# Kernel tuning notes

Hardware: AMD Instinct MI355X
Metric: run time of the kernel (lower is better)

The kernel has to match this reference:

```python
import jax, jax.numpy as jnp
import numpy as np
import math

B, N, F = 16, 1024, 2048


def setup_inputs() -> dict:
    key = jax.random.key(0)
    k_t, k_y = jax.random.split(key)
    # sorted time samples in [0, 100) per batch row
    t = jnp.sort(jax.random.uniform(k_t, (B, N), dtype=jnp.float32) * 100.0, axis=-1)
    y = jax.random.normal(k_y, (B, N), dtype=jnp.float32)
    mask = jnp.ones((B, N), dtype=jnp.float32)
    # monotonically increasing frequency grid (torch.diff in norm requires this)
    freqs = jnp.linspace(1e-5, 5.0, F, dtype=jnp.float32)
    return {"t": t, "y": y, "mask": mask, "freqs": freqs}


def reference(t, y, mask, freqs):
    # t, y, mask: (B, N); freqs: (F,)
    two_pi = 2.0 * math.pi
    omega = two_pi * freqs  # (F,)
    w = omega[None, :, None]          # (1, F, 1)
    tb = t[:, None, :]                # (B, 1, N)
    mb = mask[:, None, :]             # (B, 1, N)
    yb = y[:, None, :]                # (B, 1, N)

    # --- stage 1: tau per (batch, freq) ---
    two_wt = 2.0 * w * tb             # (B, F, N)
    s_sum = jnp.sum(jnp.sin(two_wt) * mb, axis=-1)  # (B, F)
    c_sum = jnp.sum(jnp.cos(two_wt) * mb, axis=-1)  # (B, F)
    tau = jnp.arctan2(s_sum, c_sum) / (2.0 * omega)  # (B, F)

    # --- stage 2: power ---
    wt_tau = w * (tb - tau[:, :, None])  # (B, F, N)
    cos_term = jnp.cos(wt_tau) * mb
    sin_term = jnp.sin(wt_tau) * mb
    p_cos = jnp.sum(yb * cos_term, axis=-1) ** 2 / (jnp.sum(cos_term * cos_term, axis=-1) + 1e-10)
    p_sin = jnp.sum(yb * sin_term, axis=-1) ** 2 / (jnp.sum(sin_term * sin_term, axis=-1) + 1e-10)
    p = 0.5 * (p_cos + p_sin)  # (B, F)

    # --- FAP weighting ---
    m = p.shape[-1]
    fap = 1.0 - (1.0 - jnp.exp(-p)) ** m
    p = p * (1.0 / (fap + 1e-5))

    # --- trapezoidal normalization over the freq grid ---
    df = jnp.diff(freqs)  # (F-1,)
    integral = jnp.sum(0.5 * (p[:, :-1] + p[:, 1:]) * df, axis=-1) + 1e-10  # (B,)
    return p / integral[:, None]
```

## Files before the change

### kernel.cpp

```cpp
#include <hip/hip_runtime.h>
#include <math.h>

#define B_ 16
#define N_ 1024
#define F_ 2048
#define FPB 64
#define SLICES 16
#define NS (N_ / SLICES)
#define NC (NS / 4)

typedef float v2f __attribute__((ext_vector_type(2)));

__global__ __launch_bounds__(1024, 8) void ls_power_kernel(
    const float* __restrict__ t,
    const float* __restrict__ y,
    const float* __restrict__ mask,
    const float* __restrict__ freqs,
    float* __restrict__ p_out)
{
    const int tid   = threadIdx.x;
    const int fi    = tid & (FPB - 1);
    const int slice = tid >> 6;
    const int b     = blockIdx.y;
    const int f     = blockIdx.x * FPB + fi;

    const float freq = freqs[f];
    const v2f  fq2  = {freq, freq};
    const v2f  onev = {1.0f, 1.0f};
    const v2f  ntwo = {-2.0f, -2.0f};

    __shared__ float4 sh[3 * (N_ / 4)];
    if (tid < 3 * (N_ / 4)) {
        const int a = tid >> 8;
        const int i = tid & (N_ / 4 - 1);
        const float4* __restrict__ src =
            (a == 0) ? (const float4*)t : (a == 1) ? (const float4*)y
                                                   : (const float4*)mask;
        sh[tid] = src[b * (N_ / 4) + i];
    }

    __shared__ float red[SLICES][7][FPB];
    __syncthreads();

    const float4* __restrict__ sh_t = sh;
    const float4* __restrict__ sh_y = sh + (N_ / 4);
    const float4* __restrict__ sh_m = sh + 2 * (N_ / 4);
    const int c0 = slice * NC;

    v2f S = {0.f, 0.f}, C = S, S2 = S, C2 = S, Sy = S, Cy = S, M2 = S;

    auto pair = [&](float ta, float tb, float ya, float yb, float ma, float mb) {
        v2f tn = {ta, tb}, yn = {ya, yb}, mn = {ma, mb};
        v2f ph = fq2 * tn;
        v2f pe = __builtin_elementwise_fma(fq2, tn, -ph);
        v2f fr = {__builtin_amdgcn_fractf(ph.x),
                  __builtin_amdgcn_fractf(ph.y)};
        v2f r  = fr + pe;
        v2f s0 = {__builtin_amdgcn_sinf(r.x), __builtin_amdgcn_sinf(r.y)};
        v2f c0v = {__builtin_amdgcn_cosf(r.x), __builtin_amdgcn_cosf(r.y)};
        v2f t1 = s0 * c0v;
        v2f s2v = t1 + t1;
        v2f w  = s0 * s0;
        v2f c2v = __builtin_elementwise_fma(w, ntwo, onev);
        v2f m2v = mn * mn;
        v2f ymv = yn * mn;
        S  = __builtin_elementwise_fma(s2v, mn,  S);
        C  = __builtin_elementwise_fma(c2v, mn,  C);
        S2 = __builtin_elementwise_fma(s2v, m2v, S2);
        C2 = __builtin_elementwise_fma(c2v, m2v, C2);
        Sy = __builtin_elementwise_fma(s0,  ymv, Sy);
        Cy = __builtin_elementwise_fma(c0v, ymv, Cy);
        M2 = M2 + m2v;
    };

#pragma unroll 2
    for (int ch = 0; ch < NC; ++ch) {
        float4 tv = sh_t[c0 + ch];
        float4 yv = sh_y[c0 + ch];
        float4 mv = sh_m[c0 + ch];
        pair(tv.x, tv.y, yv.x, yv.y, mv.x, mv.y);
        pair(tv.z, tv.w, yv.z, yv.w, mv.z, mv.w);
    }

    red[slice][0][fi] = S.x  + S.y;
    red[slice][1][fi] = C.x  + C.y;
    red[slice][2][fi] = S2.x + S2.y;
    red[slice][3][fi] = C2.x + C2.y;
    red[slice][4][fi] = Sy.x + Sy.y;
    red[slice][5][fi] = Cy.x + Cy.y;
    red[slice][6][fi] = M2.x + M2.y;
    __syncthreads();

    if (slice == 0) {
        float rS = 0.f, rC = 0.f, rS2 = 0.f, rC2 = 0.f, rSy = 0.f, rCy = 0.f, rM2 = 0.f;
#pragma unroll
        for (int k = 0; k < SLICES; ++k) {
            rS  += red[k][0][fi];
            rC  += red[k][1][fi];
            rS2 += red[k][2][fi];
            rC2 += red[k][3][fi];
            rSy += red[k][4][fi];
            rCy += red[k][5][fi];
            rM2 += red[k][6][fi];
        }

        float h      = sqrtf(__builtin_fmaf(rS, rS, rC * rC)) + 1e-30f;
        float cos2p  = rC / h;
        float sin2p  = rS / h;
        float cosp   = sqrtf(0.5f * (1.0f + cos2p));
        float sinp   = __builtin_copysignf(sqrtf(0.5f * (1.0f - cos2p)), rS);

        float YC = cosp * rCy + sinp * rSy;
        float YS = cosp * rSy - sinp * rCy;
        float cross = cos2p * rC2 + sin2p * rS2;
        float CCd = 0.5f * (rM2 + cross);
        float SSd = 0.5f * (rM2 - cross);

        float p_cos = (YC * YC) / (CCd + 1e-10f);
        float p_sin = (YS * YS) / (SSd + 1e-10f);
        float p = 0.5f * (p_cos + p_sin);

        float fap = 1.0f - powf(1.0f - expf(-p), 2048.0f);
        p = p * (1.0f / (fap + 1e-5f));

        p_out[b * F_ + f] = p;
    }
}

__global__ __launch_bounds__(256) void ls_norm_kernel(
    const float* __restrict__ freqs,
    float* __restrict__ p)
{
    const int b   = blockIdx.x;
    const int tid = threadIdx.x;
    float* __restrict__ pb = p + b * F_;

    float local = 0.0f;
    for (int j = tid; j < F_ - 1; j += 256) {
        float df = freqs[j + 1] - freqs[j];
        local += 0.5f * (pb[j] + pb[j + 1]) * df;
    }

    __shared__ float sred[256];
    sred[tid] = local;
    __syncthreads();
    for (int o = 128; o > 0; o >>= 1) {
        if (tid < o) sred[tid] += sred[tid + o];
        __syncthreads();
    }
    const float integral = sred[0] + 1e-10f;

#pragma unroll
    for (int k = 0; k < F_ / 256; ++k) {
        int j = tid + k * 256;
        pb[j] = pb[j] / integral;
    }
}

extern "C" void kernel_launch(void* const* d_in, const int* in_sizes, int n_in,
                              void* d_out, int out_size, void* d_ws, size_t ws_size,
                              hipStream_t stream) {
    const float* t     = (const float*)d_in[0];
    const float* y     = (const float*)d_in[1];
    const float* mask  = (const float*)d_in[2];
    const float* freqs = (const float*)d_in[3];
    float* out = (float*)d_out;

    dim3 grid1(F_ / FPB, B_);
    ls_power_kernel<<<grid1, 1024, 0, stream>>>(t, y, mask, freqs, out);
    ls_norm_kernel<<<B_, 256, 0, stream>>>(freqs, out);
}
```

Baseline: 79.04 us.

## Fuse normalization into power kernel via last-block atomic counter

Removes the separate normalization kernel. Each block bumps a per-batch atomic counter after writing its power values, and the last block for that batch row computes the trapezoidal integral with wave shuffles and rescales the row. The aim is to save a kernel launch and its dependency gap, at the cost of a memset launch, thread fences, and serial tail work in one block per batch.

Result: slower. 81.88 us (+3.6%).

```diff
diff --git a/kernel.cpp b/kernel.cpp
--- a/kernel.cpp
+++ b/kernel.cpp
@@ -16,7 +16,8 @@
     const float* __restrict__ y,
     const float* __restrict__ mask,
     const float* __restrict__ freqs,
-    float* __restrict__ p_out)
+    float* __restrict__ p_out,
+    unsigned* __restrict__ cnt)
 {
     const int tid   = threadIdx.x;
     const int fi    = tid & (FPB - 1);
@@ -40,6 +41,8 @@
     }
 
     __shared__ float red[SLICES][7][FPB];
+    __shared__ float sred[16];
+    __shared__ int   sh_last;
     __syncthreads();
 
     const float4* __restrict__ sh_t = sh;
@@ -125,35 +128,42 @@
 
         p_out[b * F_ + f] = p;
     }
-}
 
-__global__ __launch_bounds__(256) void ls_norm_kernel(
-    const float* __restrict__ freqs,
-    float* __restrict__ p)
-{
-    const int b   = blockIdx.x;
-    const int tid = threadIdx.x;
-    float* __restrict__ pb = p + b * F_;
+    if (tid == 0) {
+        __threadfence();
+        unsigned old = atomicAdd(cnt + b, 1u);
+        int last = (old == 32u * (F_ / FPB) / 32u - 1u);
+        sh_last = last;
+        if (last) __threadfence();
+    }
+    __syncthreads();
 
-    float local = 0.0f;
-    for (int j = tid; j < F_ - 1; j += 256) {
-        float df = freqs[j + 1] - freqs[j];
-        local += 0.5f * (pb[j] + pb[j + 1]) * df;
-    }
-
-    __shared__ float sred[256];
-    sred[tid] = local;
-    __syncthreads();
-    for (int o = 128; o > 0; o >>= 1) {
-        if (tid < o) sred[tid] += sred[tid + o];
+    if (sh_last) {
+        float* __restrict__ pb = p_out + b * F_;
+        float local = 0.0f;
+#pragma unroll
+        for (int j = tid; j < F_ - 1; j += 1024) {
+            float df = freqs[j + 1] - freqs[j];
+            local += 0.5f * (pb[j] + pb[j + 1]) * df;
+        }
+#pragma unroll
+        for (int o = 32; o > 0; o >>= 1) local += __shfl_down(local, o);
+        const int lane = tid & 63, wid = tid >> 6;
+        if (lane == 0) sred[wid] = local;
         __syncthreads();
-    }
-    const float integral = sred[0] + 1e-10f;
-
+        if (wid == 0) {
+            float v = (lane < 16) ? sred[lane] : 0.0f;
 #pragma unroll
-    for (int k = 0; k < F_ / 256; ++k) {
-        int j = tid + k * 256;
-        pb[j] = pb[j] / integral;
+            for (int o = 8; o > 0; o >>= 1) v += __shfl_down(v, o);
+            if (lane == 0) sred[0] = v + 1e-10f;
+        }
+        __syncthreads();
+        const float integral = sred[0];
+#pragma unroll
+        for (int k = 0; k < F_ / 1024; ++k) {
+            int j = tid + k * 1024;
+            pb[j] = pb[j] / integral;
+        }
     }
 }
 
@@ -165,8 +175,10 @@
     const float* mask  = (const float*)d_in[2];
     const float* freqs = (const float*)d_in[3];
     float* out = (float*)d_out;
+    unsigned* cnt = (unsigned*)d_ws;
+
+    hipMemsetAsync(d_ws, 0, 16 * sizeof(unsigned), stream);
 
     dim3 grid1(F_ / FPB, B_);
-    ls_power_kernel<<<grid1, 1024, 0, stream>>>(t, y, mask, freqs, out);
-    ls_norm_kernel<<<B_, 256, 0, stream>>>(freqs, out);
+    ls_power_kernel<<<grid1, 1024, 0, stream>>>(t, y, mask, freqs, out, cnt);
 }
```
